# Kernel optimization log

Measured on AMD Instinct MI355X. Metric: run time of the kernel, lower is better.

Reference implementation:

```python
import jax, jax.numpy as jnp
import numpy as np

N_NODES = 100000
N_EDGES = 1600000
IN_DIM, HID_DIM, OUT_DIM = 64, 64, 32


def setup_inputs() -> dict:
    key = jax.random.key(0)
    ks = jax.random.split(key, 8)
    s_in = 1.0 / np.sqrt(IN_DIM)
    s_hid = 1.0 / np.sqrt(HID_DIM)
    return {
        "x": jax.random.normal(ks[0], (N_NODES, IN_DIM), dtype=jnp.float32),
        "edge_index": jax.random.randint(ks[1], (2, N_EDGES), 0, N_NODES, dtype=jnp.int64),
        "W1l": jax.random.uniform(ks[2], (IN_DIM, HID_DIM), jnp.float32, -s_in, s_in),
        "b1l": jnp.zeros((HID_DIM,), jnp.float32),
        "W1r": jax.random.uniform(ks[3], (IN_DIM, HID_DIM), jnp.float32, -s_in, s_in),
        "W2l": jax.random.uniform(ks[4], (HID_DIM, OUT_DIM), jnp.float32, -s_hid, s_hid),
        "b2l": jnp.zeros((OUT_DIM,), jnp.float32),
        "W2r": jax.random.uniform(ks[5], (HID_DIM, OUT_DIM), jnp.float32, -s_hid, s_hid),
    }


def sage_conv(x, src, dst, W_l, b_l, W_r, n_nodes):
    # PyG SAGEConv (aggr='mean'): lin_l(mean of neighbor msgs) + lin_r(x)
    msg = x[src]                                                    # [E, d] gather
    agg = jax.ops.segment_sum(msg, dst, num_segments=n_nodes)      # [N, d] scatter-add
    deg = jax.ops.segment_sum(jnp.ones_like(dst, dtype=x.dtype), dst,
                              num_segments=n_nodes)
    agg = agg / jnp.maximum(deg, 1.0)[:, None]                     # mean (0 for isolated)
    return agg @ W_l + b_l + x @ W_r


def reference(x, edge_index, W1l, b1l, W1r, W2l, b2l, W2r):
    src, dst = edge_index[0], edge_index[1]
    n = x.shape[0]
    h = jax.nn.relu(sage_conv(x, src, dst, W1l, b1l, W1r, n))
    return sage_conv(h, src, dst, W2l, b2l, W2r, n)
```

## Files before the change

### kernel.cpp

```cpp
#include <hip/hip_runtime.h>

#define N_NODES 100000
#define N_EDGES 1600000
#define B2_SHIFT 9
#define BUCK_N (1 << B2_SHIFT)
#define NB2 ((N_NODES + BUCK_N - 1) >> B2_SHIFT)
#define BCAP 9216
#define PAIR_EPB 2048
#define PAIR_BLOCKS ((N_EDGES + PAIR_EPB - 1) / PAIR_EPB)

typedef __attribute__((ext_vector_type(8))) short bf16x8;
typedef __attribute__((ext_vector_type(4))) float f32x4;

__device__ __forceinline__ unsigned pack2(float a, float b) {
    unsigned ua = __float_as_uint(a), ub = __float_as_uint(b);
    ua = (ua + 0x7FFFu + ((ua >> 16) & 1u)) >> 16;
    ub = (ub + 0x7FFFu + ((ub >> 16) & 1u)) >> 16;
    return ua | (ub << 16);
}
__device__ __forceinline__ float lo16(unsigned u) { return __uint_as_float(u << 16); }
__device__ __forceinline__ float hi16(unsigned u) { return __uint_as_float(u & 0xFFFF0000u); }

__global__ __launch_bounds__(256) void k_cast(const float* __restrict__ x,
                                              unsigned* __restrict__ xh)
{
    int i = blockIdx.x * 256 + threadIdx.x;
    if (i < N_NODES * 32) {
        float2 v = ((const float2*)x)[i];
        xh[i] = pack2(v.x, v.y);
    }
}

__global__ __launch_bounds__(256) void k_initcur(int* __restrict__ bcur)
{
    if (threadIdx.x < NB2) bcur[threadIdx.x] = threadIdx.x * BCAP;
}

__global__ __launch_bounds__(256) void k_pairs(const int* __restrict__ ei,
                                               int* __restrict__ bcur,
                                               int* __restrict__ pairs)
{
    __shared__ int lh[NB2];
    __shared__ int lbase[NB2];
    for (int i = threadIdx.x; i < NB2; i += 256) lh[i] = 0;
    __syncthreads();
    int base = blockIdx.x * PAIR_EPB;
    int myb[8], myr[8], myp[8];
#pragma unroll
    for (int t = 0; t < 8; t++) {
        int e = base + t * 256 + threadIdx.x;
        myb[t] = -1;
        if (e < N_EDGES) {
            int dst = ei[N_EDGES + e];
            int b = dst >> B2_SHIFT;
            myb[t] = b;
            myr[t] = atomicAdd(&lh[b], 1);
            myp[t] = (ei[e] << B2_SHIFT) | (dst & (BUCK_N - 1));
        }
    }
    __syncthreads();
    for (int i = threadIdx.x; i < NB2; i += 256)
        lbase[i] = lh[i] ? atomicAdd(&bcur[i], lh[i]) : 0;
    __syncthreads();
#pragma unroll
    for (int t = 0; t < 8; t++) {
        if (myb[t] >= 0) {
            int slot = lbase[myb[t]] + myr[t];
            if (slot < (myb[t] + 1) * BCAP)
                pairs[slot] = myp[t];
        }
    }
}

__global__ __launch_bounds__(512) void k_sortb(const int* __restrict__ bcur,
                                               const int* __restrict__ pairs,
                                               int* __restrict__ sorted_src,
                                               int* __restrict__ rs,
                                               int* __restrict__ re)
{
    __shared__ int lcnt[BUCK_N];
    __shared__ int lofs[BUCK_N];
    int b = blockIdx.x;
    int beg = b * BCAP, end = bcur[b];
    lcnt[threadIdx.x] = 0;
    __syncthreads();
    for (int i = beg + threadIdx.x; i < end; i += 512)
        atomicAdd(&lcnt[pairs[i] & (BUCK_N - 1)], 1);
    __syncthreads();
    int v = lcnt[threadIdx.x];
    lofs[threadIdx.x] = v;
    __syncthreads();
    for (int off = 1; off < BUCK_N; off <<= 1) {
        int t = (threadIdx.x >= off) ? lofs[threadIdx.x - off] : 0;
        __syncthreads();
        lofs[threadIdx.x] += t;
        __syncthreads();
    }
    int excl = lofs[threadIdx.x] - v;
    int n = (b << B2_SHIFT) + threadIdx.x;
    if (n < N_NODES) { rs[n] = beg + excl; re[n] = beg + excl + v; }
    lcnt[threadIdx.x] = excl;
    __syncthreads();
    for (int i = beg + threadIdx.x; i < end; i += 512) {
        int p = pairs[i];
        int idx = atomicAdd(&lcnt[p & (BUCK_N - 1)], 1);
        sorted_src[beg + idx] = p >> B2_SHIFT;
    }
}

__global__ __launch_bounds__(256) void k_agg1(const int* __restrict__ rs,
                                              const int* __restrict__ re,
                                              const int* __restrict__ sorted_src,
                                              const unsigned* __restrict__ xh,
                                              unsigned* __restrict__ agg1h)
{
    int node = blockIdx.x * 8 + (threadIdx.x >> 5);
    if (node >= N_NODES) return;
    int d2 = threadIdx.x & 31;
    int beg = rs[node], end = re[node];
    float a0 = 0.f, a1 = 0.f, b0 = 0.f, b1 = 0.f;
    int idx = beg;
    for (; idx + 4 <= end; idx += 4) {
        int s0 = sorted_src[idx], s1 = sorted_src[idx + 1];
        int s2 = sorted_src[idx + 2], s3 = sorted_src[idx + 3];
        unsigned p0 = xh[(size_t)s0 * 32 + d2];
        unsigned p1 = xh[(size_t)s1 * 32 + d2];
        unsigned p2 = xh[(size_t)s2 * 32 + d2];
        unsigned p3 = xh[(size_t)s3 * 32 + d2];
        a0 += lo16(p0) + lo16(p1);  a1 += hi16(p0) + hi16(p1);
        b0 += lo16(p2) + lo16(p3);  b1 += hi16(p2) + hi16(p3);
    }
    for (; idx < end; idx++) {
        unsigned p = xh[(size_t)sorted_src[idx] * 32 + d2];
        a0 += lo16(p);  a1 += hi16(p);
    }
    agg1h[(size_t)node * 32 + d2] = pack2(a0 + b0, a1 + b1);
}

#define TPW 2
#define NTILE ((N_NODES + 15) / 16)
#define NODE_BLOCKS (((NTILE + TPW - 1) / TPW + 3) / 4)
__global__ __launch_bounds__(256) void k_node_mfma(
    const unsigned* __restrict__ xh, const unsigned* __restrict__ agg1h,
    const int* __restrict__ rs, const int* __restrict__ re,
    const float* __restrict__ W1l, const float* __restrict__ b1l,
    const float* __restrict__ W1r, const float* __restrict__ W2l,
    const float* __restrict__ W2r,
    unsigned* __restrict__ t2h, float* __restrict__ t3)
{
    __shared__ uint4 sWF[24 * 64];
    __shared__ float sH[4][16 * 68];
    __shared__ float sT[4][16 * 44];

    for (int s = threadIdx.x; s < 1536; s += 256) {
        int f = s >> 6, l = s & 63;
        int m = l & 15, q = l >> 4;
        float w[8];
        if (f < 16) {
            int jt = f >> 2, ks = f & 3;
            int j = jt * 16 + m;
            int k0 = ks * 32 + q * 8;
#pragma unroll
            for (int i = 0; i < 8; i++) {
                int kk = k0 + i;
                w[i] = (kk < 64) ? W1l[kk * 64 + j] : W1r[(kk - 64) * 64 + j];
            }
        } else {
            int f2 = f - 16;
            int jt = f2 >> 1, ks = f2 & 1;
            int j = jt * 16 + m;
            int k0 = ks * 32 + q * 8;
#pragma unroll
            for (int i = 0; i < 8; i++) {
                int kk = k0 + i;
                w[i] = (j < 32) ? W2l[kk * 32 + j] : W2r[kk * 32 + (j - 32)];
            }
        }
        sWF[f * 64 + l] = make_uint4(pack2(w[0], w[1]), pack2(w[2], w[3]),
                                     pack2(w[4], w[5]), pack2(w[6], w[7]));
    }
    __syncthreads();

    int w = threadIdx.x >> 6, lane = threadIdx.x & 63;
    int m = lane & 15, q = lane >> 4;

    bf16x8 WF1[4][4], WF2[4][2];
#pragma unroll
    for (int jt = 0; jt < 4; jt++) {
#pragma unroll
        for (int ks = 0; ks < 4; ks++)
            WF1[jt][ks] = __builtin_bit_cast(bf16x8, sWF[(jt * 4 + ks) * 64 + lane]);
#pragma unroll
        for (int ks = 0; ks < 2; ks++)
            WF2[jt][ks] = __builtin_bit_cast(bf16x8, sWF[(16 + jt * 2 + ks) * 64 + lane]);
    }
    float bias[4];
#pragma unroll
    for (int jt = 0; jt < 4; jt++) bias[jt] = b1l[jt * 16 + m];

    float* myH = &sH[w][0];
    float* myT = &sT[w][0];
    int gw = blockIdx.x * 4 + w;

    for (int t = 0; t < TPW; t++) {
        int tile = gw * TPW + t;
        if (tile >= NTILE) break;
        int nb = tile * 16;

        int nc = nb + m; if (nc >= N_NODES) nc = N_NODES - 1;
        const uint4* arow = (const uint4*)(agg1h + (size_t)nc * 32);
        const uint4* xrow = (const uint4*)(xh + (size_t)nc * 32);
        bf16x8 AM[2], AX[2];
        AM[0] = __builtin_bit_cast(bf16x8, arow[q]);
        AM[1] = __builtin_bit_cast(bf16x8, arow[4 + q]);
        AX[0] = __builtin_bit_cast(bf16x8, xrow[q]);
        AX[1] = __builtin_bit_cast(bf16x8, xrow[4 + q]);

        float invr[4];
#pragma unroll
        for (int r = 0; r < 4; r++) {
            int nn = nb + q * 4 + r;
            int nc2 = (nn < N_NODES) ? nn : 0;
            invr[r] = 1.0f / fmaxf((float)(re[nc2] - rs[nc2]), 1.0f);
        }

#pragma unroll
        for (int jt = 0; jt < 4; jt++) {
            f32x4 aM = {0.f, 0.f, 0.f, 0.f}, aX = {0.f, 0.f, 0.f, 0.f};
            aM = __builtin_amdgcn_mfma_f32_16x16x32_bf16(AM[0], WF1[jt][0], aM, 0, 0, 0);
            aM = __builtin_amdgcn_mfma_f32_16x16x32_bf16(AM[1], WF1[jt][1], aM, 0, 0, 0);
            aX = __builtin_amdgcn_mfma_f32_16x16x32_bf16(AX[0], WF1[jt][2], aX, 0, 0, 0);
            aX = __builtin_amdgcn_mfma_f32_16x16x32_bf16(AX[1], WF1[jt][3], aX, 0, 0, 0);
#pragma unroll
            for (int r = 0; r < 4; r++) {
                float hv = fmaxf(aM[r] * invr[r] + aX[r] + bias[jt], 0.0f);
                myH[(q * 4 + r) * 68 + jt * 16 + m] = hv;
            }
        }

        bf16x8 A2[2];
#pragma unroll
        for (int ks = 0; ks < 2; ks++) {
            const float* p = &myH[m * 68 + ks * 32 + q * 8];
            float4 v0 = *(const float4*)p;
            float4 v1 = *(const float4*)(p + 4);
            uint4 u = make_uint4(pack2(v0.x, v0.y), pack2(v0.z, v0.w),
                                 pack2(v1.x, v1.y), pack2(v1.z, v1.w));
            A2[ks] = __builtin_bit_cast(bf16x8, u);
        }

#pragma unroll
        for (int jt = 0; jt < 4; jt++) {
            f32x4 acc = {0.f, 0.f, 0.f, 0.f};
            acc = __builtin_amdgcn_mfma_f32_16x16x32_bf16(A2[0], WF2[jt][0], acc, 0, 0, 0);
            acc = __builtin_amdgcn_mfma_f32_16x16x32_bf16(A2[1], WF2[jt][1], acc, 0, 0, 0);
            if (jt < 2) {
#pragma unroll
                for (int r = 0; r < 4; r++)
                    myT[(q * 4 + r) * 44 + jt * 16 + m] = acc[r];
            } else {
#pragma unroll
                for (int r = 0; r < 4; r++) {
                    int nn = nb + q * 4 + r;
                    if (nn < N_NODES)
                        t3[(size_t)nn * 32 + (jt - 2) * 16 + m] = acc[r];
                }
            }
        }

        int ni = lane >> 2, u4g = lane & 3;
        const float* tp = &myT[ni * 44 + u4g * 8];
        float4 a = *(const float4*)tp;
        float4 b = *(const float4*)(tp + 4);
        if (nb + ni < N_NODES) {
            uint4 o = make_uint4(pack2(a.x, a.y), pack2(a.z, a.w),
                                 pack2(b.x, b.y), pack2(b.z, b.w));
            *(uint4*)(t2h + (size_t)(nb + ni) * 16 + u4g * 4) = o;
        }
    }
}

__global__ __launch_bounds__(256) void k_agg2out(
    const int* __restrict__ rs, const int* __restrict__ re,
    const int* __restrict__ sorted_src,
    const unsigned* __restrict__ t2h, const float* __restrict__ t3,
    const float* __restrict__ b2l, float* __restrict__ out)
{
    int node = blockIdx.x * 16 + (threadIdx.x >> 4);
    if (node >= N_NODES) return;
    int d2 = threadIdx.x & 15;
    int beg = rs[node], end = re[node];
    float a0 = 0.f, a1 = 0.f, b0 = 0.f, b1 = 0.f;
    int idx = beg;
    for (; idx + 4 <= end; idx += 4) {
        int s0 = sorted_src[idx], s1 = sorted_src[idx + 1];
        int s2 = sorted_src[idx + 2], s3 = sorted_src[idx + 3];
        unsigned p0 = t2h[(size_t)s0 * 16 + d2];
        unsigned p1 = t2h[(size_t)s1 * 16 + d2];
        unsigned p2 = t2h[(size_t)s2 * 16 + d2];
        unsigned p3 = t2h[(size_t)s3 * 16 + d2];
        a0 += lo16(p0) + lo16(p1);  a1 += hi16(p0) + hi16(p1);
        b0 += lo16(p2) + lo16(p3);  b1 += hi16(p2) + hi16(p3);
    }
    for (; idx < end; idx++) {
        unsigned p = t2h[(size_t)sorted_src[idx] * 16 + d2];
        a0 += lo16(p);  a1 += hi16(p);
    }
    float inv = 1.0f / fmaxf((float)(end - beg), 1.0f);
    float2 tv = ((const float2*)(t3 + (size_t)node * 32))[d2];
    float2 bv = ((const float2*)b2l)[d2];
    ((float2*)(out + (size_t)node * 32))[d2] =
        make_float2((a0 + b0) * inv + tv.x + bv.x,
                    (a1 + b1) * inv + tv.y + bv.y);
}

extern "C" void kernel_launch(void* const* d_in, const int* in_sizes, int n_in,
                              void* d_out, int out_size, void* d_ws, size_t ws_size,
                              hipStream_t stream) {
    const float* x   = (const float*)d_in[0];
    const int*   ei  = (const int*)d_in[1];
    const float* W1l = (const float*)d_in[2];
    const float* b1l = (const float*)d_in[3];
    const float* W1r = (const float*)d_in[4];
    const float* W2l = (const float*)d_in[5];
    const float* b2l = (const float*)d_in[6];
    const float* W2r = (const float*)d_in[7];
    float* out = (float*)d_out;

    const size_t N = N_NODES;
    int* wsi = (int*)d_ws;
    int*      pairs      = wsi;
    int*      sorted_src = wsi + 1806336;
    int*      bcur       = wsi + 3612672;
    int*      rs         = wsi + 3612928;
    int*      re         = wsi + 3712928;
    unsigned* xh         = (unsigned*)(wsi + 3812928);
    unsigned* t2h        = xh + 32 * N;
    unsigned* agg1h      = t2h + 16 * N;
    float*    t3         = (float*)(agg1h + 32 * N);

    k_cast   <<<(int)((N * 32 + 255) / 256), 256, 0, stream>>>(x, xh);
    k_initcur<<<1, 256, 0, stream>>>(bcur);
    k_pairs  <<<PAIR_BLOCKS, 256, 0, stream>>>(ei, bcur, pairs);
    k_sortb  <<<NB2, 512, 0, stream>>>(bcur, pairs, sorted_src, rs, re);

    k_agg1     <<<(int)((N + 7) / 8), 256, 0, stream>>>(rs, re, sorted_src, xh, agg1h);
    k_node_mfma<<<NODE_BLOCKS, 256, 0, stream>>>(xh, agg1h, rs, re,
                                                 W1l, b1l, W1r, W2l, W2r, t2h, t3);
    k_agg2out  <<<(int)((N + 15) / 16), 256, 0, stream>>>(rs, re, sorted_src,
                                                 t2h, t3, b2l, out);
}
```

Before: 221.9 us.

## Split pair histogram, use wave-shuffle scan, and unroll gather loops to eight

The pair-binning kernel now handles 4096 edges per block and keeps two shared-memory histograms, chosen by wave parity, to halve LDS atomic contention. The bucket sort replaces its barrier-heavy LDS Hillis-Steele scan with a wave-level shuffle scan plus a small cross-wave sum. Both aggregation kernels unroll their neighbour gather to eight loads in flight, with a pairwise tail loop. Larger blocks raise register pressure and leave fewer blocks, and the deeper unroll adds registers per thread.

```diff
diff --git a/kernel.cpp b/kernel.cpp
--- a/kernel.cpp
+++ b/kernel.cpp
@@ -6,7 +6,7 @@
 #define BUCK_N (1 << B2_SHIFT)
 #define NB2 ((N_NODES + BUCK_N - 1) >> B2_SHIFT)
 #define BCAP 9216
-#define PAIR_EPB 2048
+#define PAIR_EPB 4096
 #define PAIR_BLOCKS ((N_EDGES + PAIR_EPB - 1) / PAIR_EPB)
 
 typedef __attribute__((ext_vector_type(8))) short bf16x8;
@@ -40,32 +40,37 @@
                                                int* __restrict__ bcur,
                                                int* __restrict__ pairs)
 {
-    __shared__ int lh[NB2];
-    __shared__ int lbase[NB2];
-    for (int i = threadIdx.x; i < NB2; i += 256) lh[i] = 0;
-    __syncthreads();
+    __shared__ int lh[2][NB2];
+    __shared__ int lb[2][NB2];
+    for (int i = threadIdx.x; i < NB2; i += 256) { lh[0][i] = 0; lh[1][i] = 0; }
+    __syncthreads();
+    int cp = (threadIdx.x >> 6) & 1;
     int base = blockIdx.x * PAIR_EPB;
-    int myb[8], myr[8], myp[8];
-#pragma unroll
-    for (int t = 0; t < 8; t++) {
+    int myb[16], myr[16], myp[16];
+#pragma unroll
+    for (int t = 0; t < 16; t++) {
         int e = base + t * 256 + threadIdx.x;
         myb[t] = -1;
         if (e < N_EDGES) {
             int dst = ei[N_EDGES + e];
             int b = dst >> B2_SHIFT;
             myb[t] = b;
-            myr[t] = atomicAdd(&lh[b], 1);
+            myr[t] = atomicAdd(&lh[cp][b], 1);
             myp[t] = (ei[e] << B2_SHIFT) | (dst & (BUCK_N - 1));
         }
     }
     __syncthreads();
-    for (int i = threadIdx.x; i < NB2; i += 256)
-        lbase[i] = lh[i] ? atomicAdd(&bcur[i], lh[i]) : 0;
-    __syncthreads();
-#pragma unroll
-    for (int t = 0; t < 8; t++) {
+    for (int i = threadIdx.x; i < NB2; i += 256) {
+        int c0 = lh[0][i], c1 = lh[1][i];
+        int basei = (c0 + c1) ? atomicAdd(&bcur[i], c0 + c1) : 0;
+        lb[0][i] = basei;
+        lb[1][i] = basei + c0;
+    }
+    __syncthreads();
+#pragma unroll
+    for (int t = 0; t < 16; t++) {
         if (myb[t] >= 0) {
-            int slot = lbase[myb[t]] + myr[t];
+            int slot = lb[cp][myb[t]] + myr[t];
             if (slot < (myb[t] + 1) * BCAP)
                 pairs[slot] = myp[t];
         }
@@ -79,7 +84,7 @@
                                                int* __restrict__ re)
 {
     __shared__ int lcnt[BUCK_N];
-    __shared__ int lofs[BUCK_N];
+    __shared__ int wtot[8];
     int b = blockIdx.x;
     int beg = b * BCAP, end = bcur[b];
     lcnt[threadIdx.x] = 0;
@@ -88,23 +93,28 @@
         atomicAdd(&lcnt[pairs[i] & (BUCK_N - 1)], 1);
     __syncthreads();
     int v = lcnt[threadIdx.x];
-    lofs[threadIdx.x] = v;
-    __syncthreads();
-    for (int off = 1; off < BUCK_N; off <<= 1) {
-        int t = (threadIdx.x >= off) ? lofs[threadIdx.x - off] : 0;
-        __syncthreads();
-        lofs[threadIdx.x] += t;
-        __syncthreads();
-    }
-    int excl = lofs[threadIdx.x] - v;
+    int lane = threadIdx.x & 63, wid = threadIdx.x >> 6;
+    int s = v;
+#pragma unroll
+    for (int off = 1; off < 64; off <<= 1) {
+        int t = __shfl_up(s, off);
+        if (lane >= off) s += t;
+    }
+    if (lane == 63) wtot[wid] = s;
+    __syncthreads();
+    int woff = 0;
+#pragma unroll
+    for (int k = 0; k < 8; k++) woff += (k < wid) ? wtot[k] : 0;
+    int excl = woff + s - v;
     int n = (b << B2_SHIFT) + threadIdx.x;
     if (n < N_NODES) { rs[n] = beg + excl; re[n] = beg + excl + v; }
-    lcnt[threadIdx.x] = excl;
+    __syncthreads();
+    lcnt[threadIdx.x] = beg + excl;
     __syncthreads();
     for (int i = beg + threadIdx.x; i < end; i += 512) {
         int p = pairs[i];
         int idx = atomicAdd(&lcnt[p & (BUCK_N - 1)], 1);
-        sorted_src[beg + idx] = p >> B2_SHIFT;
+        sorted_src[idx] = p >> B2_SHIFT;
     }
 }
 
@@ -120,17 +130,31 @@
     int beg = rs[node], end = re[node];
     float a0 = 0.f, a1 = 0.f, b0 = 0.f, b1 = 0.f;
     int idx = beg;
-    for (; idx + 4 <= end; idx += 4) {
-        int s0 = sorted_src[idx], s1 = sorted_src[idx + 1];
+    for (; idx + 8 <= end; idx += 8) {
+        int s0 = sorted_src[idx + 0], s1 = sorted_src[idx + 1];
         int s2 = sorted_src[idx + 2], s3 = sorted_src[idx + 3];
+        int s4 = sorted_src[idx + 4], s5 = sorted_src[idx + 5];
+        int s6 = sorted_src[idx + 6], s7 = sorted_src[idx + 7];
         unsigned p0 = xh[(size_t)s0 * 32 + d2];
         unsigned p1 = xh[(size_t)s1 * 32 + d2];
         unsigned p2 = xh[(size_t)s2 * 32 + d2];
         unsigned p3 = xh[(size_t)s3 * 32 + d2];
+        unsigned p4 = xh[(size_t)s4 * 32 + d2];
+        unsigned p5 = xh[(size_t)s5 * 32 + d2];
+        unsigned p6 = xh[(size_t)s6 * 32 + d2];
+        unsigned p7 = xh[(size_t)s7 * 32 + d2];
         a0 += lo16(p0) + lo16(p1);  a1 += hi16(p0) + hi16(p1);
         b0 += lo16(p2) + lo16(p3);  b1 += hi16(p2) + hi16(p3);
-    }
-    for (; idx < end; idx++) {
+        a0 += lo16(p4) + lo16(p5);  a1 += hi16(p4) + hi16(p5);
+        b0 += lo16(p6) + lo16(p7);  b1 += hi16(p6) + hi16(p7);
+    }
+    for (; idx + 2 <= end; idx += 2) {
+        int s0 = sorted_src[idx], s1 = sorted_src[idx + 1];
+        unsigned p0 = xh[(size_t)s0 * 32 + d2];
+        unsigned p1 = xh[(size_t)s1 * 32 + d2];
+        a0 += lo16(p0) + lo16(p1);  a1 += hi16(p0) + hi16(p1);
+    }
+    if (idx < end) {
         unsigned p = xh[(size_t)sorted_src[idx] * 32 + d2];
         a0 += lo16(p);  a1 += hi16(p);
     }
@@ -292,17 +316,31 @@
     int beg = rs[node], end = re[node];
     float a0 = 0.f, a1 = 0.f, b0 = 0.f, b1 = 0.f;
     int idx = beg;
-    for (; idx + 4 <= end; idx += 4) {
-        int s0 = sorted_src[idx], s1 = sorted_src[idx + 1];
+    for (; idx + 8 <= end; idx += 8) {
+        int s0 = sorted_src[idx + 0], s1 = sorted_src[idx + 1];
         int s2 = sorted_src[idx + 2], s3 = sorted_src[idx + 3];
+        int s4 = sorted_src[idx + 4], s5 = sorted_src[idx + 5];
+        int s6 = sorted_src[idx + 6], s7 = sorted_src[idx + 7];
         unsigned p0 = t2h[(size_t)s0 * 16 + d2];
         unsigned p1 = t2h[(size_t)s1 * 16 + d2];
         unsigned p2 = t2h[(size_t)s2 * 16 + d2];
         unsigned p3 = t2h[(size_t)s3 * 16 + d2];
+        unsigned p4 = t2h[(size_t)s4 * 16 + d2];
+        unsigned p5 = t2h[(size_t)s5 * 16 + d2];
+        unsigned p6 = t2h[(size_t)s6 * 16 + d2];
+        unsigned p7 = t2h[(size_t)s7 * 16 + d2];
         a0 += lo16(p0) + lo16(p1);  a1 += hi16(p0) + hi16(p1);
         b0 += lo16(p2) + lo16(p3);  b1 += hi16(p2) + hi16(p3);
-    }
-    for (; idx < end; idx++) {
+        a0 += lo16(p4) + lo16(p5);  a1 += hi16(p4) + hi16(p5);
+        b0 += lo16(p6) + lo16(p7);  b1 += hi16(p6) + hi16(p7);
+    }
+    for (; idx + 2 <= end; idx += 2) {
+        int s0 = sorted_src[idx], s1 = sorted_src[idx + 1];
+        unsigned p0 = t2h[(size_t)s0 * 16 + d2];
+        unsigned p1 = t2h[(size_t)s1 * 16 + d2];
+        a0 += lo16(p0) + lo16(p1);  a1 += hi16(p0) + hi16(p1);
+    }
+    if (idx < end) {
         unsigned p = t2h[(size_t)sorted_src[idx] * 16 + d2];
         a0 += lo16(p);  a1 += hi16(p);
     }
```

Result: faster. 208.1 us (-6.2%).
